# Optimization experiments

Hardware: AMD Instinct MI355X
Metric: run time of the kernel (lower is better)

## Reference

```python
import jax, jax.numpy as jnp
import numpy as np

N_E = 16384
SPLIT = (512, 512)
BETA = 0.25
K = 10
B = 4096


def _l2n(x):
    # F.normalize(p=2, dim=-1)
    return x * jax.lax.rsqrt(jnp.sum(x * x, axis=-1, keepdims=True) + 1e-12)


def _dist(x, y):
    return (jnp.sum(x * x, axis=1, keepdims=True)
            + jnp.sum(y * y, axis=1)
            - 2.0 * jnp.einsum('bd,nd->bn', x, y))


def _usage(idx):
    counts = jnp.zeros((N_E,), jnp.float32).at[idx.reshape(-1)].add(1.0)
    return jnp.sum(counts > 0).astype(jnp.float32) / N_E


def _soft_topk(d, emb):
    # smallest-K distances -> softmax(-values) weighted codebook mix
    neg_vals, idx = jax.lax.top_k(-d, K)            # [B, K]
    w = jax.nn.softmax(neg_vals, axis=1)            # softmax(-values)
    z_q = jnp.einsum('bk,bkd->bd', w, emb[idx])     # gather + weighted sum
    return z_q, idx


def _losses(z_q, z):
    vq = jnp.mean((z_q - jax.lax.stop_gradient(z)) ** 2)
    commit = BETA * jnp.mean((jax.lax.stop_gradient(z_q) - z) ** 2)
    return vq, commit


def setup_inputs() -> dict:
    key = jax.random.key(0)
    ks = jax.random.split(key, 5)
    u = 1.0 / N_E
    return {
        'z': jax.random.normal(ks[0], (B, sum(SPLIT)), jnp.float32),
        'w_text': jax.random.uniform(ks[1], (N_E, SPLIT[0]), jnp.float32, -u, u),
        'w_graph': jax.random.uniform(ks[2], (N_E, SPLIT[1]), jnp.float32, -u, u),
        'w_shared_text': jax.random.uniform(ks[3], (N_E, SPLIT[0]), jnp.float32, -u, u),
        'w_shared_graph': jax.random.uniform(ks[4], (N_E, SPLIT[1]), jnp.float32, -u, u),
    }


def reference(z, w_text, w_graph, w_shared_text, w_shared_graph):
    z_text, z_graph = jnp.split(z, [SPLIT[0]], axis=-1)

    # ---- shared codebook (joint text+graph distance) ----
    zt_n, zg_n = _l2n(z_text), _l2n(z_graph)
    wst_n, wsg_n = _l2n(w_shared_text), _l2n(w_shared_graph)
    d_shared = _dist(zt_n, wst_n) + 1.0 * _dist(zg_n, wsg_n)
    shared_emb = jnp.concatenate([wst_n, wsg_n], axis=-1)
    zq_s, idx_s = _soft_topk(d_shared, shared_emb)
    vq_s, com_s = _losses(zq_s, z)
    zq_s = z + jax.lax.stop_gradient(zq_s - z)      # straight-through
    usage_s = _usage(idx_s)

    # ---- text-specific codebook ----
    wt_n = _l2n(w_text)
    d_t = _dist(zt_n, wt_n)
    zq_t, idx_t = _soft_topk(d_t, wt_n)
    vq_t, com_t = _losses(zq_t, z_text)
    zq_t = z_text + jax.lax.stop_gradient(zq_t - z_text)
    usage_t = _usage(idx_t)

    # ---- graph-specific codebook ----
    wg_n = _l2n(w_graph)
    d_g = _dist(zg_n, wg_n)
    zq_g, idx_g = _soft_topk(d_g, wg_n)
    vq_g, com_g = _losses(zq_g, z_graph)
    zq_g = z_graph + jax.lax.stop_gradient(zq_g - z_graph)
    usage_g = _usage(idx_g)

    shared_text_emb, shared_graph_emb = jnp.split(zq_s, [SPLIT[0]], axis=-1)
    return (zq_s, shared_text_emb, shared_graph_emb, zq_t, zq_g,
            vq_s, com_s, vq_t, com_t, vq_g, com_g,
            usage_s, usage_t, usage_g)
```

## Files before the change

### kernel.cpp

```cpp
#include <hip/hip_runtime.h>
#include <stdint.h>

#define NE      16384
#define BATCH   4096
#define DFULL   1024
#define DHALF   512
#define TOPK    10
#define NCHUNK  16
#define CHUNK   1024
#define CPC     40
#define NCAND   (NCHUNK * CPC)
#define MRES    24
#define BETA_C  0.25f

#define O1 ((size_t)BATCH * DFULL)
#define O2 (O1 + (size_t)BATCH * DHALF)
#define O3 (O2 + (size_t)BATCH * DHALF)
#define O4 (O3 + (size_t)BATCH * DHALF)
#define O5 (O4 + (size_t)BATCH * DHALF)

typedef __bf16 bf16x8 __attribute__((ext_vector_type(8)));
typedef float  f32x4  __attribute__((ext_vector_type(4)));

__device__ inline uint16_t f2bf(float f) {
    unsigned u = __float_as_uint(f);
    unsigned r = (u + 0x7FFFu + ((u >> 16) & 1u)) >> 16;
    return (uint16_t)r;
}
__device__ inline float bf2f(uint16_t u) {
    return __uint_as_float(((unsigned)u) << 16);
}

__device__ inline float dot4(float4 a, float4 b) {
    return a.x*b.x + a.y*b.y + a.z*b.z + a.w*b.w;
}

__global__ __launch_bounds__(256) void k_norm_z(const float* __restrict__ z,
                                                uint16_t* __restrict__ zn,
                                                float* __restrict__ rnzt,
                                                float* __restrict__ rnzg) {
    int b = blockIdx.x, t = threadIdx.x;
    const float4* zp = (const float4*)(z + (size_t)b * DFULL);
    float4 v = zp[t];
    float ss = v.x*v.x + v.y*v.y + v.z*v.z + v.w*v.w;
    #pragma unroll
    for (int off = 32; off; off >>= 1) ss += __shfl_xor(ss, off);
    __shared__ float red[4];
    if ((t & 63) == 0) red[t >> 6] = ss;
    __syncthreads();
    float tot = (t < 128) ? (red[0] + red[1]) : (red[2] + red[3]);
    float rn = rsqrtf(tot + 1e-12f);
    if (t == 0)   rnzt[b] = rn;
    if (t == 128) rnzg[b] = rn;
    uint16_t* o = zn + (size_t)b * DFULL + t * 4;
    o[0] = f2bf(v.x * rn); o[1] = f2bf(v.y * rn);
    o[2] = f2bf(v.z * rn); o[3] = f2bf(v.w * rn);
}

__global__ __launch_bounds__(128) void k_norm_cb(const float* __restrict__ w,
                                                 uint16_t* __restrict__ dst, int dstld,
                                                 float* __restrict__ rns) {
    int r = blockIdx.x, t = threadIdx.x;
    const float4* wp = (const float4*)(w + (size_t)r * DHALF);
    float4 v = wp[t];
    float ss = v.x*v.x + v.y*v.y + v.z*v.z + v.w*v.w;
    #pragma unroll
    for (int off = 32; off; off >>= 1) ss += __shfl_xor(ss, off);
    __shared__ float red[2];
    if ((t & 63) == 0) red[t >> 6] = ss;
    __syncthreads();
    float rn = rsqrtf(red[0] + red[1] + 1e-12f);
    if (t == 0) rns[r] = rn;
    uint16_t* o = dst + (size_t)r * dstld + t * 4;
    o[0] = f2bf(v.x * rn); o[1] = f2bf(v.y * rn);
    o[2] = f2bf(v.z * rn); o[3] = f2bf(v.w * rn);
}

__global__ __launch_bounds__(256, 3) void k_gemm_topk(
    const uint16_t* __restrict__ Zn, int ldz, int zoff,
    const uint16_t* __restrict__ Wn, int ldw, int KT,
    unsigned* __restrict__ cand)
{
    __shared__ uint16_t Wsm[2][128 * 64];
    __shared__ uint16_t Zsm[2][64 * 64];

    const int tid  = threadIdx.x;
    const int lane = tid & 63;
    const int wv   = tid >> 6;
    const int wr   = wv >> 1;
    const int wc   = wv & 1;
    const int q    = lane >> 4;
    const int c    = lane & 15;
    const int rowbase  = blockIdx.y * 64;
    const int entchunk = blockIdx.x * CHUNK;

    int so0, so1, so2, so3, so4, so5;
    int lo0, lo1, lo2, lo3, lo4, lo5;
    {
        int o, row, kb;
        o = (0 * 4 + wv) * 1024 + lane * 16; row = o >> 7; kb = (o & 127) ^ ((row & 7) << 4);
        so0 = row * (ldw * 2) + kb; lo0 = o;
        o = (1 * 4 + wv) * 1024 + lane * 16; row = o >> 7; kb = (o & 127) ^ ((row & 7) << 4);
        so1 = row * (ldw * 2) + kb; lo1 = o;
        o = (2 * 4 + wv) * 1024 + lane * 16; row = o >> 7; kb = (o & 127) ^ ((row & 7) << 4);
        so2 = row * (ldw * 2) + kb; lo2 = o;
        o = (3 * 4 + wv) * 1024 + lane * 16; row = o >> 7; kb = (o & 127) ^ ((row & 7) << 4);
        so3 = row * (ldw * 2) + kb; lo3 = o;
        o = (0 * 4 + wv) * 1024 + lane * 16; row = o >> 7; kb = (o & 127) ^ ((row & 7) << 4);
        so4 = row * (ldz * 2) + kb; lo4 = o;
        o = (1 * 4 + wv) * 1024 + lane * 16; row = o >> 7; kb = (o & 127) ^ ((row & 7) << 4);
        so5 = row * (ldz * 2) + kb; lo5 = o;
    }

    const char* Wbase = (const char*)Wn;
    const char* Zbase = (const char*)(Zn + zoff);

    unsigned La0 = 0, La1 = 0, La2 = 0, La3 = 0, La4 = 0;
    unsigned Lb0 = 0, Lb1 = 0, Lb2 = 0, Lb3 = 0, Lb4 = 0;

    uint4 sw0, sw1, sw2, sw3, sz0, sz1;

#define LOADG(cb2, kt2) {                                                           \
        const char* Wg = Wbase + ((size_t)(entchunk + (cb2) * 128) * ldw + (kt2) * 64) * 2; \
        const char* Zg = Zbase + ((size_t)rowbase * ldz + (kt2) * 64) * 2;          \
        sw0 = *(const uint4*)(Wg + so0);                                            \
        sw1 = *(const uint4*)(Wg + so1);                                            \
        sw2 = *(const uint4*)(Wg + so2);                                            \
        sw3 = *(const uint4*)(Wg + so3);                                            \
        sz0 = *(const uint4*)(Zg + so4);                                            \
        sz1 = *(const uint4*)(Zg + so5);                                            \
    }
#define WRITES(bufi) {                                                              \
        char* Wd = (char*)&Wsm[bufi][0];                                            \
        char* Zd = (char*)&Zsm[bufi][0];                                            \
        *(uint4*)(Wd + lo0) = sw0;                                                  \
        *(uint4*)(Wd + lo1) = sw1;                                                  \
        *(uint4*)(Wd + lo2) = sw2;                                                  \
        *(uint4*)(Wd + lo3) = sw3;                                                  \
        *(uint4*)(Zd + lo4) = sz0;                                                  \
        *(uint4*)(Zd + lo5) = sz1;                                                  \
    }

    LOADG(0, 0);
    WRITES(0);
    __syncthreads();
    int cur = 0;

    for (int cb = 0; cb < 8; ++cb) {
        f32x4 acc[4][2];
        #pragma unroll
        for (int m = 0; m < 4; ++m)
            #pragma unroll
            for (int n = 0; n < 2; ++n)
                acc[m][n] = (f32x4){0.f, 0.f, 0.f, 0.f};

        for (int kt = 0; kt < KT; ++kt) {
            int last = (kt + 1 == KT);
            int ncb = last ? cb + 1 : cb;
            int nkt = last ? 0 : kt + 1;
            int havenext = (ncb < 8);
            if (havenext) LOADG(ncb, nkt);

            const char* Wb = (const char*)&Wsm[cur][0];
            const char* Zb = (const char*)&Zsm[cur][0];
            #pragma unroll
            for (int ks = 0; ks < 2; ++ks) {
                int kb = ks * 64 + q * 16;
                bf16x8 b[2];
                #pragma unroll
                for (int n = 0; n < 2; ++n) {
                    int rb = wc * 32 + n * 16 + c;
                    b[n] = *(const bf16x8*)(Zb + rb * 128 + (kb ^ ((rb & 7) << 4)));
                }
                #pragma unroll
                for (int m = 0; m < 4; ++m) {
                    int ra = wr * 64 + m * 16 + c;
                    bf16x8 a = *(const bf16x8*)(Wb + ra * 128 + (kb ^ ((ra & 7) << 4)));
                    #pragma unroll
                    for (int n = 0; n < 2; ++n)
                        acc[m][n] = __builtin_amdgcn_mfma_f32_16x16x32_bf16(
                                        a, b[n], acc[m][n], 0, 0, 0);
                }
            }

            if (havenext) WRITES(cur ^ 1);
            __syncthreads();
            cur ^= 1;
        }

        const int entbase = entchunk + cb * 128 + wr * 64 + q * 4;
        #pragma unroll
        for (int n = 0; n < 2; ++n) {
            #pragma unroll
            for (int m = 0; m < 4; ++m) {
                #pragma unroll
                for (int i = 0; i < 4; ++i) {
                    unsigned u  = __float_as_uint(acc[m][n][i]);
                    unsigned mg = (unsigned)((int)u >> 31);
                    unsigned h  = (u >> 16) ^ (mg | 0x8000u);
                    unsigned p  = (h << 16) | (unsigned)(entbase + m * 16 + i);
                    if (n == 0) {
                        bool g0 = p > La0, g1 = p > La1, g2 = p > La2,
                             g3 = p > La3, g4 = p > La4;
                        La4 = g4 ? (g3 ? La3 : p) : La4;
                        La3 = g3 ? (g2 ? La2 : p) : La3;
                        La2 = g2 ? (g1 ? La1 : p) : La2;
                        La1 = g1 ? (g0 ? La0 : p) : La1;
                        La0 = g0 ? p : La0;
                    } else {
                        bool g0 = p > Lb0, g1 = p > Lb1, g2 = p > Lb2,
                             g3 = p > Lb3, g4 = p > Lb4;
                        Lb4 = g4 ? (g3 ? Lb3 : p) : Lb4;
                        Lb3 = g3 ? (g2 ? Lb2 : p) : Lb3;
                        Lb2 = g2 ? (g1 ? Lb1 : p) : Lb2;
                        Lb1 = g1 ? (g0 ? Lb0 : p) : Lb1;
                        Lb0 = g0 ? p : Lb0;
                    }
                }
            }
        }
    }

    {
        int grow = rowbase + wc * 32 + 0 * 16 + c;
        unsigned* dst = cand + ((size_t)grow * NCHUNK + blockIdx.x) * CPC + wr * 20 + q * 5;
        dst[0] = La0; dst[1] = La1; dst[2] = La2; dst[3] = La3; dst[4] = La4;
        grow = rowbase + wc * 32 + 1 * 16 + c;
        dst = cand + ((size_t)grow * NCHUNK + blockIdx.x) * CPC + wr * 20 + q * 5;
        dst[0] = Lb0; dst[1] = Lb1; dst[2] = Lb2; dst[3] = Lb3; dst[4] = Lb4;
    }
#undef LOADG
#undef WRITES
}

__global__ __launch_bounds__(256) void k_merge_all(
    const unsigned* __restrict__ cand,
    const uint16_t* __restrict__ wshn, const uint16_t* __restrict__ wtn,
    const uint16_t* __restrict__ wgn,
    const float* __restrict__ w_st, const float* __restrict__ w_sg,
    const float* __restrict__ w_t,  const float* __restrict__ w_g,
    const float* __restrict__ rnst, const float* __restrict__ rnsg,
    const float* __restrict__ rnt,  const float* __restrict__ rng,
    const float* __restrict__ rnzt, const float* __restrict__ rnzg,
    const float* __restrict__ z, float* __restrict__ out,
    unsigned int* __restrict__ bm, float* __restrict__ ls)
{
    const int b = blockIdx.x, g = blockIdx.y, tid = threadIdx.x;
    const int lane = tid & 63, wv = tid >> 6;

    const unsigned* cd; const uint16_t* emb;
    const float *w0, *w1, *rn0, *rn1, *rz0p, *rz1p;
    int zoff, ld;
    float *outm, *outs1, *outs2;
    if (g == 0) {
        cd = cand;                      emb = wshn;
        w0 = w_st; w1 = w_sg; rn0 = rnst; rn1 = rnsg; rz0p = rnzt; rz1p = rnzg;
        zoff = 0;   ld = DFULL;
        outm = out; outs1 = out + O1; outs2 = out + O2;
    } else if (g == 1) {
        cd = cand + (size_t)BATCH * NCAND;     emb = wtn;
        w0 = w_t; w1 = nullptr; rn0 = rnt; rn1 = nullptr; rz0p = rnzt; rz1p = nullptr;
        zoff = 0;   ld = DHALF;
        outm = out + O3; outs1 = nullptr; outs2 = nullptr;
    } else {
        cd = cand + (size_t)2 * BATCH * NCAND; emb = wgn;
        w0 = w_g; w1 = nullptr; rn0 = rng; rn1 = nullptr; rz0p = rnzg; rz1p = nullptr;
        zoff = 512; ld = DHALF;
        outm = out + O4; outs1 = nullptr; outs2 = nullptr;
    }
    unsigned int* bitmap = bm + g * (NE / 32);
    float* lossacc = ls + g;

    __shared__ float zsh[DFULL];
    __shared__ unsigned scand[MRES];
    __shared__ float ssh[MRES];
    __shared__ float wts[TOPK];
    __shared__ int   ish[TOPK];
    __shared__ float serr[4];

    const float* zrow = z + (size_t)b * DFULL + zoff;
    for (int cc = tid; cc < ld / 4; cc += 256)
        ((float4*)zsh)[cc] = ((const float4*)zrow)[cc];

    if (wv == 0) {
        unsigned creg[10];
        const unsigned* cb_ = cd + (size_t)b * NCAND;
        #pragma unroll
        for (int j = 0; j < 10; ++j) creg[j] = cb_[lane + 64 * j];
        for (int k = 0; k < MRES; ++k) {
            unsigned bv = 0;
            #pragma unroll
            for (int j = 0; j < 10; ++j) bv = (creg[j] > bv) ? creg[j] : bv;
            #pragma unroll
            for (int off = 32; off; off >>= 1) {
                unsigned ov = __shfl_xor(bv, off);
                bv = (ov > bv) ? ov : bv;
            }
            #pragma unroll
            for (int j = 0; j < 10; ++j) if (creg[j] == bv) creg[j] = 0u;
            if (lane == 0) scand[k] = bv;
        }
    }
    __syncthreads();

    const float rz0 = rz0p[b];
    const float rz1 = w1 ? rz1p[b] : 0.f;
    const float4* z4 = (const float4*)zsh;
    for (int cc = wv; cc < MRES; cc += 4) {
        int idx = scand[cc] & 0xFFFFu;
        const float4* wr0 = (const float4*)(w0 + (size_t)idx * DHALF);
        float d0 = dot4(wr0[lane], z4[lane]) + dot4(wr0[64 + lane], z4[64 + lane]);
        float s = d0 * (rz0 * rn0[idx]);
        if (w1) {
            const float4* wr1 = (const float4*)(w1 + (size_t)idx * DHALF);
        float d1 = dot4(wr1[lane], z4[128 + lane]) + dot4(wr1[64 + lane], z4[192 + lane]);
            s += d1 * (rz1 * rn1[idx]);
        }
        #pragma unroll
        for (int off = 32; off; off >>= 1) s += __shfl_xor(s, off);
        if (lane == 0) ssh[cc] = s;
    }
    __syncthreads();

    if (wv == 0) {
        float val = (lane < MRES) ? ssh[lane] : -1e30f;
        float vk[TOPK]; int sk[TOPK];
        #pragma unroll
        for (int k = 0; k < TOPK; ++k) {
            float v = val; int who = lane;
            #pragma unroll
            for (int off = 32; off; off >>= 1) {
                float ov = __shfl_xor(v, off);
                int   ow = __shfl_xor(who, off);
                if (ov > v || (ov == v && ow < who)) { v = ov; who = ow; }
            }
            vk[k] = v; sk[k] = who;
            if (lane == who) val = -1e30f;
        }
        if (lane == 0) {
            float vmax = vk[0], e[TOPK], sum = 0.f;
            #pragma unroll
            for (int k = 0; k < TOPK; ++k) { e[k] = expf(2.f * (vk[k] - vmax)); sum += e[k]; }
            #pragma unroll
            for (int k = 0; k < TOPK; ++k) {
                float w = e[k] / sum;
                int idx = scand[sk[k]] & 0xFFFFu;
                ish[k] = idx;
                wts[k] = w;
                atomicOr(&bitmap[idx >> 5], 1u << (idx & 31));
            }
        }
    }
    __syncthreads();

    float wk[TOPK]; int ik[TOPK];
    #pragma unroll
    for (int k = 0; k < TOPK; ++k) { wk[k] = wts[k]; ik[k] = ish[k]; }

    float err = 0.f;
    const int ng = ld / 4;
    for (int g2 = tid; g2 < ng; g2 += 256) {
        float ax = 0.f, ay = 0.f, az = 0.f, aw = 0.f;
        #pragma unroll
        for (int k = 0; k < TOPK; ++k) {
            ushort4 e = ((const ushort4*)(emb + (size_t)ik[k] * ld))[g2];
            float wv_ = wk[k];
            ax += wv_ * bf2f(e.x); ay += wv_ * bf2f(e.y);
            az += wv_ * bf2f(e.z); aw += wv_ * bf2f(e.w);
        }
        float4 zz = ((const float4*)zsh)[g2];
        float dx = ax - zz.x, dy = ay - zz.y, dz_ = az - zz.z, dw = aw - zz.w;
        err += dx*dx + dy*dy + dz_*dz_ + dw*dw;
        float4 a4 = {ax, ay, az, aw};
        ((float4*)(outm + (size_t)b * ld))[g2] = a4;
        if (outs1) {
            if (g2 < 128) ((float4*)(outs1 + (size_t)b * DHALF))[g2] = a4;
            else          ((float4*)(outs2 + (size_t)b * DHALF))[g2 - 128] = a4;
        }
    }
    #pragma unroll
    for (int off = 32; off; off >>= 1) err += __shfl_xor(err, off);
    if (lane == 0) serr[wv] = err;
    __syncthreads();
    if (tid == 0) atomicAdd(lossacc, serr[0] + serr[1] + serr[2] + serr[3]);
}

__global__ __launch_bounds__(256) void k_scalars(const unsigned int* __restrict__ bm,
                                                 const float* __restrict__ lossacc,
                                                 float* __restrict__ out)
{
    __shared__ float red[4];
    int tid = threadIdx.x;
    float counts[3];
    for (int g = 0; g < 3; ++g) {
        unsigned c = 0;
        for (int w = tid; w < NE / 32; w += 256) c += __popc(bm[g * (NE / 32) + w]);
        float f = (float)c;
        #pragma unroll
        for (int off = 32; off; off >>= 1) f += __shfl_xor(f, off);
        if ((tid & 63) == 0) red[tid >> 6] = f;
        __syncthreads();
        counts[g] = red[0] + red[1] + red[2] + red[3];
        __syncthreads();
    }
    if (tid == 0) {
        float vq_s = lossacc[0] / (4096.f * 1024.f);
        float vq_t = lossacc[1] / (4096.f * 512.f);
        float vq_g = lossacc[2] / (4096.f * 512.f);
        out[0] = vq_s; out[1] = BETA_C * vq_s;
        out[2] = vq_t; out[3] = BETA_C * vq_t;
        out[4] = vq_g; out[5] = BETA_C * vq_g;
        out[6] = counts[0] / (float)NE;
        out[7] = counts[1] / (float)NE;
        out[8] = counts[2] / (float)NE;
    }
}

extern "C" void kernel_launch(void* const* d_in, const int* in_sizes, int n_in,
                              void* d_out, int out_size, void* d_ws, size_t ws_size,
                              hipStream_t stream) {
    const float* z    = (const float*)d_in[0];
    const float* w_t  = (const float*)d_in[1];
    const float* w_g  = (const float*)d_in[2];
    const float* w_st = (const float*)d_in[3];
    const float* w_sg = (const float*)d_in[4];
    float* out = (float*)d_out;

    uint8_t* ws = (uint8_t*)d_ws;
    const size_t OFF_ZN  = 0;
    const size_t OFF_WSH = OFF_ZN  + (size_t)BATCH * DFULL * 2;
    const size_t OFF_WT  = OFF_WSH + (size_t)NE * DFULL * 2;
    const size_t OFF_WG  = OFF_WT  + (size_t)NE * DHALF * 2;
    const size_t OFF_CD  = OFF_WG  + (size_t)NE * DHALF * 2;
    const size_t OFF_RN  = OFF_CD  + (size_t)3 * BATCH * NCAND * 4;
    const size_t OFF_RNZ = OFF_RN  + (size_t)4 * NE * 4;
    const size_t OFF_BM  = OFF_RNZ + (size_t)2 * BATCH * 4;
    const size_t OFF_LS  = OFF_BM  + (size_t)3 * (NE / 8);

    uint16_t* zn   = (uint16_t*)(ws + OFF_ZN);
    uint16_t* wsh  = (uint16_t*)(ws + OFF_WSH);
    uint16_t* wt   = (uint16_t*)(ws + OFF_WT);
    uint16_t* wg   = (uint16_t*)(ws + OFF_WG);
    unsigned* cd   = (unsigned*)(ws + OFF_CD);
    float*    rnst = (float*)(ws + OFF_RN);
    float*    rnsg = rnst + NE;
    float*    rnt  = rnsg + NE;
    float*    rng  = rnt + NE;
    float*    rnzt = (float*)(ws + OFF_RNZ);
    float*    rnzg = rnzt + BATCH;
    unsigned* bm   = (unsigned*)(ws + OFF_BM);
    float*    ls   = (float*)(ws + OFF_LS);

    hipMemsetAsync(ws + OFF_BM, 0, 3 * (NE / 8) + 64, stream);

    k_norm_z<<<BATCH, 256, 0, stream>>>(z, zn, rnzt, rnzg);
    k_norm_cb<<<NE, 128, 0, stream>>>(w_st, wsh,        DFULL, rnst);
    k_norm_cb<<<NE, 128, 0, stream>>>(w_sg, wsh + 512,  DFULL, rnsg);
    k_norm_cb<<<NE, 128, 0, stream>>>(w_t,  wt,         DHALF, rnt);
    k_norm_cb<<<NE, 128, 0, stream>>>(w_g,  wg,         DHALF, rng);

    const size_t CD1 = (size_t)BATCH * NCAND;
    dim3 gg(NCHUNK, BATCH / 64);
    k_gemm_topk<<<gg, 256, 0, stream>>>(zn, DFULL, 0,   wsh, DFULL, 16, cd);
    k_gemm_topk<<<gg, 256, 0, stream>>>(zn, DFULL, 0,   wt,  DHALF,  8, cd + CD1);
    k_gemm_topk<<<gg, 256, 0, stream>>>(zn, DFULL, 512, wg,  DHALF,  8, cd + 2 * CD1);

    k_merge_all<<<dim3(BATCH, 3), 256, 0, stream>>>(
        cd, wsh, wt, wg,
        w_st, w_sg, w_t, w_g,
        rnst, rnsg, rnt, rng,
        rnzt, rnzg,
        z, out, bm, ls);

    k_scalars<<<1, 256, 0, stream>>>(bm, ls, out + O5);
}
```

Baseline: 736.1 us.

## Merge norm and gemm launches; rescore candidates from bf16 normalized codebooks

Combines the four codebook normalization launches into one grid and the three gemm+topk launches into one 3D grid, cutting launch gaps and tail idle time. The candidate rescoring in the merge kernel now reads the already-normalized bf16 codebook rows instead of the fp32 originals plus per-row norms, halving the bytes gathered per candidate. The cost is lower precision on the codebook side of the exact rescore, which may perturb the top-k ordering and the softmax weights.

```diff
diff --git a/kernel.cpp b/kernel.cpp
--- a/kernel.cpp
+++ b/kernel.cpp
@@ -12,6 +12,7 @@
 #define NCAND   (NCHUNK * CPC)
 #define MRES    24
 #define BETA_C  0.25f
+#define CD1     ((size_t)BATCH * NCAND)
 
 #define O1 ((size_t)BATCH * DFULL)
 #define O2 (O1 + (size_t)BATCH * DHALF)
@@ -30,9 +31,17 @@
 __device__ inline float bf2f(uint16_t u) {
     return __uint_as_float(((unsigned)u) << 16);
 }
-
-__device__ inline float dot4(float4 a, float4 b) {
-    return a.x*b.x + a.y*b.y + a.z*b.z + a.w*b.w;
+__device__ inline float dot8bf(uint4 e, const float* zp) {
+    float s;
+    s  = __uint_as_float(e.x << 16)          * zp[0];
+    s += __uint_as_float(e.x & 0xFFFF0000u)  * zp[1];
+    s += __uint_as_float(e.y << 16)          * zp[2];
+    s += __uint_as_float(e.y & 0xFFFF0000u)  * zp[3];
+    s += __uint_as_float(e.z << 16)          * zp[4];
+    s += __uint_as_float(e.z & 0xFFFF0000u)  * zp[5];
+    s += __uint_as_float(e.w << 16)          * zp[6];
+    s += __uint_as_float(e.w & 0xFFFF0000u)  * zp[7];
+    return s;
 }
 
 __global__ __launch_bounds__(256) void k_norm_z(const float* __restrict__ z,
@@ -57,10 +66,17 @@
     o[2] = f2bf(v.z * rn); o[3] = f2bf(v.w * rn);
 }
 
-__global__ __launch_bounds__(128) void k_norm_cb(const float* __restrict__ w,
-                                                 uint16_t* __restrict__ dst, int dstld,
-                                                 float* __restrict__ rns) {
-    int r = blockIdx.x, t = threadIdx.x;
+__global__ __launch_bounds__(128) void k_norm_cb_all(
+    const float* __restrict__ w_st, const float* __restrict__ w_sg,
+    const float* __restrict__ w_t,  const float* __restrict__ w_g,
+    uint16_t* __restrict__ wsh, uint16_t* __restrict__ wt, uint16_t* __restrict__ wg,
+    float* __restrict__ rns ) {
+    int r = blockIdx.x, t = threadIdx.x, y = blockIdx.y;
+    const float* w; uint16_t* dst; int dstld; float* rn_;
+    if (y == 0)      { w = w_st; dst = wsh;       dstld = DFULL; rn_ = rns; }
+    else if (y == 1) { w = w_sg; dst = wsh + 512; dstld = DFULL; rn_ = rns + NE; }
+    else if (y == 2) { w = w_t;  dst = wt;        dstld = DHALF; rn_ = rns + 2 * NE; }
+    else             { w = w_g;  dst = wg;        dstld = DHALF; rn_ = rns + 3 * NE; }
     const float4* wp = (const float4*)(w + (size_t)r * DHALF);
     float4 v = wp[t];
     float ss = v.x*v.x + v.y*v.y + v.z*v.z + v.w*v.w;
@@ -70,15 +86,16 @@
     if ((t & 63) == 0) red[t >> 6] = ss;
     __syncthreads();
     float rn = rsqrtf(red[0] + red[1] + 1e-12f);
-    if (t == 0) rns[r] = rn;
+    if (t == 0) rn_[r] = rn;
     uint16_t* o = dst + (size_t)r * dstld + t * 4;
     o[0] = f2bf(v.x * rn); o[1] = f2bf(v.y * rn);
     o[2] = f2bf(v.z * rn); o[3] = f2bf(v.w * rn);
 }
 
 __global__ __launch_bounds__(256, 3) void k_gemm_topk(
-    const uint16_t* __restrict__ Zn, int ldz, int zoff,
-    const uint16_t* __restrict__ Wn, int ldw, int KT,
+    const uint16_t* __restrict__ Zn,
+    const uint16_t* __restrict__ wshn, const uint16_t* __restrict__ wtn,
+    const uint16_t* __restrict__ wgn,
     unsigned* __restrict__ cand)
 {
     __shared__ uint16_t Wsm[2][128 * 64];
@@ -93,6 +110,13 @@
     const int c    = lane & 15;
     const int rowbase  = blockIdx.y * 64;
     const int entchunk = blockIdx.x * CHUNK;
+    const int gz = blockIdx.z;
+
+    const uint16_t* Wn; int ldw, KT, zoff; unsigned* cdst;
+    if (gz == 0)      { Wn = wshn; ldw = DFULL; KT = 16; zoff = 0;   cdst = cand; }
+    else if (gz == 1) { Wn = wtn;  ldw = DHALF; KT = 8;  zoff = 0;   cdst = cand + CD1; }
+    else              { Wn = wgn;  ldw = DHALF; KT = 8;  zoff = 512; cdst = cand + 2 * CD1; }
+    const int ldz = DFULL;
 
     int so0, so1, so2, so3, so4, so5;
     int lo0, lo1, lo2, lo3, lo4, lo5;
@@ -223,10 +247,10 @@
 
     {
         int grow = rowbase + wc * 32 + 0 * 16 + c;
-        unsigned* dst = cand + ((size_t)grow * NCHUNK + blockIdx.x) * CPC + wr * 20 + q * 5;
+        unsigned* dst = cdst + ((size_t)grow * NCHUNK + blockIdx.x) * CPC + wr * 20 + q * 5;
         dst[0] = La0; dst[1] = La1; dst[2] = La2; dst[3] = La3; dst[4] = La4;
         grow = rowbase + wc * 32 + 1 * 16 + c;
-        dst = cand + ((size_t)grow * NCHUNK + blockIdx.x) * CPC + wr * 20 + q * 5;
+        dst = cdst + ((size_t)grow * NCHUNK + blockIdx.x) * CPC + wr * 20 + q * 5;
         dst[0] = Lb0; dst[1] = Lb1; dst[2] = Lb2; dst[3] = Lb3; dst[4] = Lb4;
     }
 #undef LOADG
@@ -237,10 +261,6 @@
     const unsigned* __restrict__ cand,
     const uint16_t* __restrict__ wshn, const uint16_t* __restrict__ wtn,
     const uint16_t* __restrict__ wgn,
-    const float* __restrict__ w_st, const float* __restrict__ w_sg,
-    const float* __restrict__ w_t,  const float* __restrict__ w_g,
-    const float* __restrict__ rnst, const float* __restrict__ rnsg,
-    const float* __restrict__ rnt,  const float* __restrict__ rng,
     const float* __restrict__ rnzt, const float* __restrict__ rnzg,
     const float* __restrict__ z, float* __restrict__ out,
     unsigned int* __restrict__ bm, float* __restrict__ ls)
@@ -249,24 +269,21 @@
     const int lane = tid & 63, wv = tid >> 6;
 
     const unsigned* cd; const uint16_t* emb;
-    const float *w0, *w1, *rn0, *rn1, *rz0p, *rz1p;
     int zoff, ld;
     float *outm, *outs1, *outs2;
+    float rz0, rz1;
     if (g == 0) {
-        cd = cand;                      emb = wshn;
-        w0 = w_st; w1 = w_sg; rn0 = rnst; rn1 = rnsg; rz0p = rnzt; rz1p = rnzg;
-        zoff = 0;   ld = DFULL;
+        cd = cand;           emb = wshn; zoff = 0;   ld = DFULL;
         outm = out; outs1 = out + O1; outs2 = out + O2;
+        rz0 = rnzt[b]; rz1 = rnzg[b];
     } else if (g == 1) {
-        cd = cand + (size_t)BATCH * NCAND;     emb = wtn;
-        w0 = w_t; w1 = nullptr; rn0 = rnt; rn1 = nullptr; rz0p = rnzt; rz1p = nullptr;
-        zoff = 0;   ld = DHALF;
+        cd = cand + CD1;     emb = wtn;  zoff = 0;   ld = DHALF;
         outm = out + O3; outs1 = nullptr; outs2 = nullptr;
+        rz0 = rnzt[b]; rz1 = 0.f;
     } else {
-        cd = cand + (size_t)2 * BATCH * NCAND; emb = wgn;
-        w0 = w_g; w1 = nullptr; rn0 = rng; rn1 = nullptr; rz0p = rnzg; rz1p = nullptr;
-        zoff = 512; ld = DHALF;
+        cd = cand + 2 * CD1; emb = wgn;  zoff = 512; ld = DHALF;
         outm = out + O4; outs1 = nullptr; outs2 = nullptr;
+        rz0 = rnzg[b]; rz1 = 0.f;
     }
     unsigned int* bitmap = bm + g * (NE / 32);
     float* lossacc = ls + g;
@@ -303,22 +320,18 @@
     }
     __syncthreads();
 
-    const float rz0 = rz0p[b];
-    const float rz1 = w1 ? rz1p[b] : 0.f;
-    const float4* z4 = (const float4*)zsh;
     for (int cc = wv; cc < MRES; cc += 4) {
         int idx = scand[cc] & 0xFFFFu;
-        const float4* wr0 = (const float4*)(w0 + (size_t)idx * DHALF);
-        float d0 = dot4(wr0[lane], z4[lane]) + dot4(wr0[64 + lane], z4[64 + lane]);
-        float s = d0 * (rz0 * rn0[idx]);
-        if (w1) {
-            const float4* wr1 = (const float4*)(w1 + (size_t)idx * DHALF);
-        float d1 = dot4(wr1[lane], z4[128 + lane]) + dot4(wr1[64 + lane], z4[192 + lane]);
-            s += d1 * (rz1 * rn1[idx]);
-        }
-        #pragma unroll
-        for (int off = 32; off; off >>= 1) s += __shfl_xor(s, off);
-        if (lane == 0) ssh[cc] = s;
+        const uint16_t* er = emb + (size_t)idx * ld;
+        uint4 e0 = *(const uint4*)(er + lane * 8);
+        float t = rz0 * dot8bf(e0, zsh + lane * 8);
+        if (ld == DFULL) {
+            uint4 e1 = *(const uint4*)(er + 512 + lane * 8);
+            t += rz1 * dot8bf(e1, zsh + 512 + lane * 8);
+        }
+        #pragma unroll
+        for (int off = 32; off; off >>= 1) t += __shfl_xor(t, off);
+        if (lane == 0) ssh[cc] = t;
     }
     __syncthreads();
 
@@ -442,10 +455,7 @@
     uint16_t* wt   = (uint16_t*)(ws + OFF_WT);
     uint16_t* wg   = (uint16_t*)(ws + OFF_WG);
     unsigned* cd   = (unsigned*)(ws + OFF_CD);
-    float*    rnst = (float*)(ws + OFF_RN);
-    float*    rnsg = rnst + NE;
-    float*    rnt  = rnsg + NE;
-    float*    rng  = rnt + NE;
+    float*    rns  = (float*)(ws + OFF_RN);
     float*    rnzt = (float*)(ws + OFF_RNZ);
     float*    rnzg = rnzt + BATCH;
     unsigned* bm   = (unsigned*)(ws + OFF_BM);
@@ -454,23 +464,13 @@
     hipMemsetAsync(ws + OFF_BM, 0, 3 * (NE / 8) + 64, stream);
 
     k_norm_z<<<BATCH, 256, 0, stream>>>(z, zn, rnzt, rnzg);
-    k_norm_cb<<<NE, 128, 0, stream>>>(w_st, wsh,        DFULL, rnst);
-    k_norm_cb<<<NE, 128, 0, stream>>>(w_sg, wsh + 512,  DFULL, rnsg);
-    k_norm_cb<<<NE, 128, 0, stream>>>(w_t,  wt,         DHALF, rnt);
-    k_norm_cb<<<NE, 128, 0, stream>>>(w_g,  wg,         DHALF, rng);
-
-    const size_t CD1 = (size_t)BATCH * NCAND;
-    dim3 gg(NCHUNK, BATCH / 64);
-    k_gemm_topk<<<gg, 256, 0, stream>>>(zn, DFULL, 0,   wsh, DFULL, 16, cd);
-    k_gemm_topk<<<gg, 256, 0, stream>>>(zn, DFULL, 0,   wt,  DHALF,  8, cd + CD1);
-    k_gemm_topk<<<gg, 256, 0, stream>>>(zn, DFULL, 512, wg,  DHALF,  8, cd + 2 * CD1);
+    k_norm_cb_all<<<dim3(NE, 4), 128, 0, stream>>>(w_st, w_sg, w_t, w_g,
+                                                   wsh, wt, wg, rns);
+
+    k_gemm_topk<<<dim3(NCHUNK, BATCH / 64, 3), 256, 0, stream>>>(zn, wsh, wt, wg, cd);
 
     k_merge_all<<<dim3(BATCH, 3), 256, 0, stream>>>(
-        cd, wsh, wt, wg,
-        w_st, w_sg, w_t, w_g,
-        rnst, rnsg, rnt, rng,
-        rnzt, rnzg,
-        z, out, bm, ls);
+        cd, wsh, wt, wg, rnzt, rnzg, z, out, bm, ls);
 
     k_scalars<<<1, 256, 0, stream>>>(bm, ls, out + O5);
 }
```

Result: faster. 646.9 us (-12.1%).
